# Performance work log

Hardware: AMD Instinct MI355X
Metric: run time of the kernel (lower is better)

Reference implementation:

```python
import jax, jax.numpy as jnp
import numpy as np

HIDDEN_DIM = 8


def setup_inputs() -> dict:
    key = jax.random.key(0)
    ks = jax.random.split(key, 10)
    B, S, C, H = 2048, 200, 25, HIDDEN_DIM
    s = 0.1
    return {
        "x": jax.random.normal(ks[0], (B, S, C), jnp.float32),
        "delay_W": jax.random.normal(ks[1], (S, C), jnp.float32) * s,
        "delay_b": jax.random.normal(ks[2], (S,), jnp.float32) * s,
        "U_W": jax.random.normal(ks[3], (H, C), jnp.float32) * s,
        "U_b": jax.random.normal(ks[4], (H,), jnp.float32) * s,
        "A_W": jax.random.normal(ks[5], (H, H), jnp.float32) * s,
        "B_W": jax.random.normal(ks[6], (H, C), jnp.float32) * s,
        "B_b": jax.random.normal(ks[7], (H,), jnp.float32) * s,
        "out_W": jax.random.normal(ks[8], (C, H), jnp.float32) * s,
        "out_b": jax.random.normal(ks[9], (C,), jnp.float32) * s,
    }


def reference(x, delay_W, delay_b, U_W, U_b, A_W, B_W, B_b, out_W, out_b):
    # x: [B, S, C] -> [S, B, C]
    xt = jnp.swapaxes(x, 0, 1)
    S, B, C = xt.shape
    # synaptic delay: each source timestep t distributes its signal over
    # all output timesteps via a softmax over the TIMESTEPS axis.
    logits = xt @ delay_W.T + delay_b                # [S, B, S]
    w = jax.nn.softmax(logits, axis=-1)              # [S, B, S_out]
    x_del = jnp.einsum('tbc,tbs->sbc', xt, w)        # [S_out, B, C]
    # SSM inputs
    u = x_del @ U_W.T + U_b                          # [S, B, H]
    b = jax.nn.sigmoid(x_del @ B_W.T + B_b)          # [S, B, H]

    # linear recurrence h_t = h_{t-1} A^T + b_t * u_t, h_0 = 0
    def step(h, bu):
        b_t, u_t = bu
        h = h @ A_W.T + b_t * u_t
        return h, h

    h0 = jnp.zeros((B, HIDDEN_DIM), xt.dtype)
    _, hs = jax.lax.scan(step, h0, (b, u))           # [S, B, H]
    out = hs @ out_W.T + out_b                       # [S, B, C]
    return jnp.swapaxes(out, 0, 1)                   # [B, S, C]
```

## Files before the change

kernel.cpp:

```cpp
#include <hip/hip_runtime.h>

#define NB 2048
#define S_ 200
#define C_ 25
#define H_ 8
#define WROWS 208
#define STR 36
#define NSTRIP 13
#define NSTILE 13
#define NPAIR 7
#define XDS 26
#define WFRAG (13 * 64 * 4)

typedef __bf16   bf16x8 __attribute__((ext_vector_type(8)));
typedef float    f32x4  __attribute__((ext_vector_type(4)));
typedef unsigned uint4v __attribute__((ext_vector_type(4)));

struct Frag { bf16x8 hi, lo; };

__device__ __forceinline__ unsigned short f2bf(float f) {
    unsigned u = __builtin_bit_cast(unsigned, f);
    return (unsigned short)((u + 0x7FFFu + ((u >> 16) & 1u)) >> 16);
}
__device__ __forceinline__ float bfh2f(unsigned short h) {
    return __builtin_bit_cast(float, (unsigned)h << 16);
}
__device__ __forceinline__ unsigned pack_hl(float v) {
    unsigned short h = f2bf(v);
    unsigned short l = f2bf(v - bfh2f(h));
    return (unsigned)h | ((unsigned)l << 16);
}
__device__ __forceinline__ unsigned hi_pair(unsigned d0, unsigned d1) {
    return (d0 & 0xFFFFu) | (d1 << 16);
}
__device__ __forceinline__ unsigned lo_pair(unsigned d0, unsigned d1) {
    return (d0 >> 16) | (d1 & 0xFFFF0000u);
}
__device__ __forceinline__ Frag build_frag8(uint4v d0, uint4v d1) {
    uint4v h, l;
    h.x = hi_pair(d0.x, d0.y); h.y = hi_pair(d0.z, d0.w);
    h.z = hi_pair(d1.x, d1.y); h.w = hi_pair(d1.z, d1.w);
    l.x = lo_pair(d0.x, d0.y); l.y = lo_pair(d0.z, d0.w);
    l.z = lo_pair(d1.x, d1.y); l.w = lo_pair(d1.z, d1.w);
    Frag f;
    f.hi = __builtin_bit_cast(bf16x8, h);
    f.lo = __builtin_bit_cast(bf16x8, l);
    return f;
}
__device__ __forceinline__ bf16x8 build_hi8(uint4v d0, uint4v d1) {
    uint4v h;
    h.x = hi_pair(d0.x, d0.y); h.y = hi_pair(d0.z, d0.w);
    h.z = hi_pair(d1.x, d1.y); h.w = hi_pair(d1.z, d1.w);
    return __builtin_bit_cast(bf16x8, h);
}
__device__ __forceinline__ f32x4 mfma16(bf16x8 a, bf16x8 b, f32x4 c) {
    return __builtin_amdgcn_mfma_f32_16x16x32_bf16(a, b, c, 0, 0, 0);
}
__device__ __forceinline__ f32x4 mfma_split(const Frag& a, const Frag& b, f32x4 c) {
    c = mfma16(a.hi, b.hi, c);
    c = mfma16(a.hi, b.lo, c);
    c = mfma16(a.lo, b.hi, c);
    return c;
}
__device__ __forceinline__ float fexp2(float x) {
    float r; asm("v_exp_f32 %0, %1" : "=v"(r) : "v"(x)); return r;
}
__device__ __forceinline__ float flog2(float x) {
    float r; asm("v_log_f32 %0, %1" : "=v"(r) : "v"(x)); return r;
}
__device__ __forceinline__ unsigned cvt_pk_bf16(float vlo, float vhi) {
    unsigned r; asm("v_cvt_pk_bf16_f32 %0, %1, %2" : "=v"(r) : "v"(vlo), "v"(vhi)); return r;
}
__device__ __forceinline__ float lo16f(unsigned p) { return __builtin_bit_cast(float, p << 16); }
__device__ __forceinline__ float hi16f(unsigned p) { return __builtin_bit_cast(float, p & 0xFFFF0000u); }

__device__ __forceinline__ void xpose_quads(unsigned& a0, unsigned& a1,
                                            unsigned& b0, unsigned& b1) {
    asm("v_permlane32_swap_b32 %0, %1" : "+v"(a0), "+v"(b0));
    asm("v_permlane32_swap_b32 %0, %1" : "+v"(a1), "+v"(b1));
    asm("v_permlane16_swap_b32 %0, %1" : "+v"(a0), "+v"(b0));
    asm("v_permlane16_swap_b32 %0, %1" : "+v"(a1), "+v"(b1));
}

__global__ void prep_w_kernel(const float* __restrict__ delay_W,
                              const float* __restrict__ A_W,
                              unsigned* __restrict__ ws) {
    const float LOG2E = 1.44269504088896340736f;
    unsigned* Whi = ws;
    unsigned* Wlo = ws + WFRAG;
    for (int idx = blockIdx.x * 256 + threadIdx.x; idx < WFRAG; idx += gridDim.x * 256) {
        int d = idx & 3, lane = (idx >> 2) & 63, sv = idx >> 8;
        int q = lane >> 4, nn = lane & 15;
        int s  = sv * 16 + nn;
        int c0 = q * 8 + 2 * d;
        float v0 = (s < S_ && c0     < C_) ? delay_W[s * C_ + c0]     * LOG2E : 0.f;
        float v1 = (s < S_ && c0 + 1 < C_) ? delay_W[s * C_ + c0 + 1] * LOG2E : 0.f;
        unsigned short h0 = f2bf(v0), h1 = f2bf(v1);
        unsigned short l0 = f2bf(v0 - bfh2f(h0)), l1 = f2bf(v1 - bfh2f(h1));
        Whi[idx] = (unsigned)h0 | ((unsigned)h1 << 16);
        Wlo[idx] = (unsigned)l0 | ((unsigned)l1 << 16);
    }
    __shared__ float A2s[64];
    if (blockIdx.x == 0) {
        float* A2g = (float*)(ws + 2 * WFRAG);
        float* A4g = (float*)(ws + 2 * WFRAG + 64);
        const int i = threadIdx.x >> 3, j = threadIdx.x & 7;
        if (threadIdx.x < 64) {
            float s = 0.f;
            for (int k = 0; k < 8; ++k) s = fmaf(A_W[i * 8 + k], A_W[k * 8 + j], s);
            A2s[threadIdx.x] = s; A2g[threadIdx.x] = s;
        }
        __syncthreads();
        if (threadIdx.x < 64) {
            float s = 0.f;
            for (int k = 0; k < 8; ++k) s = fmaf(A2s[i * 8 + k], A2s[k * 8 + j], s);
            A4g[threadIdx.x] = s;
        }
    }
}

__global__ __launch_bounds__(256, 5) void ssm_syn_delay_kernel(
    const float* __restrict__ x,       const unsigned* __restrict__ ws,
    const float* __restrict__ delay_b, const float* __restrict__ U_W,
    const float* __restrict__ U_b,     const float* __restrict__ A_W,
    const float* __restrict__ B_W,     const float* __restrict__ B_b,
    const float* __restrict__ out_W,   const float* __restrict__ out_b,
    float* __restrict__ out)
{
    __shared__ __align__(16) unsigned X32[WROWS * STR];
    __shared__ __align__(16) float lsed[WROWS];
    __shared__ __align__(16) float dbs_l[WROWS];

    const int tid  = threadIdx.x;
    const int wid  = tid >> 6;
    const int lane = tid & 63;
    const int q    = lane >> 4;
    const int n    = lane & 15;
    const int b    = blockIdx.x;
    const float* xb = x + (size_t)b * (S_ * C_);
    const unsigned* Whi = ws;
    const unsigned* Wlo = ws + WFRAG;
    const float* A2g = (const float*)(ws + 2 * WFRAG);
    const float* A4g = (const float*)(ws + 2 * WFRAG + 64);

    for (int i = tid; i < WROWS * 9; i += 256) {
        int r = i / 9, cg = i - r * 9;
        f32x4 v = {0.f, 0.f, 0.f, 0.f};
        if (r < S_) {
            if (cg < 6)       __builtin_memcpy(&v, &xb[r * C_ + cg * 4], 16);
            else if (cg == 6) v[0] = xb[r * C_ + 24];
        }
        uint4v p;
        p.x = pack_hl(v[0]); p.y = pack_hl(v[1]); p.z = pack_hl(v[2]); p.w = pack_hl(v[3]);
        *(uint4v*)&X32[r * STR + cg * 4] = p;
    }
    for (int i = tid; i < WROWS; i += 256)
        dbs_l[i] = (i < S_) ? delay_b[i] * 1.44269504088896340736f : -1e30f;
    __syncthreads();

    for (int st = wid; st < NSTRIP; st += 4) {
        const int t = st * 16 + n;
        const uint4v* xp = (const uint4v*)&X32[t * STR + q * 8];
        Frag fa = build_frag8(xp[0], xp[1]);
        float rs0 = 0.f, rs1 = 0.f, rs2 = 0.f, rs3 = 0.f;
        for (int sv = 0; sv < NSTILE; ++sv) {
            Frag fb;
            fb.hi = __builtin_bit_cast(bf16x8, *(const uint4v*)&Whi[(sv * 64 + lane) * 4]);
            fb.lo = __builtin_bit_cast(bf16x8, *(const uint4v*)&Wlo[(sv * 64 + lane) * 4]);
            f32x4 L = {0.f, 0.f, 0.f, 0.f};
            L = mfma_split(fa, fb, L);
            const float dbv = dbs_l[sv * 16 + n];
            rs0 += fexp2(L[0] + dbv);
            rs1 += fexp2(L[1] + dbv);
            rs2 += fexp2(L[2] + dbv);
            rs3 += fexp2(L[3] + dbv);
        }
#pragma unroll
        for (int off = 1; off < 16; off <<= 1) {
            rs0 += __shfl_xor(rs0, off);
            rs1 += __shfl_xor(rs1, off);
            rs2 += __shfl_xor(rs2, off);
            rs3 += __shfl_xor(rs3, off);
        }
        if (n < 4) {
            float v = (n == 0) ? rs0 : (n == 1) ? rs1 : (n == 2) ? rs2 : rs3;
            lsed[st * 16 + q * 4 + n] = flog2(v);
        }
    }
    __syncthreads();

    f32x4 acc[4][2];
#pragma unroll
    for (int i = 0; i < 4; ++i)
#pragma unroll
        for (int j = 0; j < 2; ++j) acc[i][j] = f32x4{0.f, 0.f, 0.f, 0.f};

    for (int pair = 0; pair < NPAIR; ++pair) {
        const int sA = 2 * pair, sB = sA + 1;
        const bool bval = (sB < NSTRIP);
        const uint4v* xpA = (const uint4v*)&X32[(sA * 16 + n) * STR + q * 8];
        Frag faA = build_frag8(xpA[0], xpA[1]);
        Frag faB;
        if (bval) {
            const uint4v* xpB = (const uint4v*)&X32[(sB * 16 + n) * STR + q * 8];
            faB = build_frag8(xpB[0], xpB[1]);
        }
        f32x4 lseA = *(const f32x4*)&lsed[sA * 16 + q * 4];
        f32x4 lseB = bval ? *(const f32x4*)&lsed[sB * 16 + q * 4] : f32x4{0,0,0,0};
        bf16x8 b2h[2];
#pragma unroll
        for (int ct = 0; ct < 2; ++ct) {
            const int c = ct * 16 + n;
            uint4v d0, d1;
#pragma unroll
            for (int j = 0; j < 4; ++j) {
                int t2 = pair * 32 + q * 8 + j;
                ((unsigned*)&d0)[j] = (t2 < WROWS) ? X32[t2 * STR + c] : 0u;
            }
#pragma unroll
            for (int j = 0; j < 4; ++j) {
                int t2 = pair * 32 + q * 8 + 4 + j;
                ((unsigned*)&d1)[j] = (t2 < WROWS) ? X32[t2 * STR + c] : 0u;
            }
            b2h[ct] = build_hi8(d0, d1);
        }

#pragma unroll
        for (int si = 0; si < 4; ++si) {
            const int sv = wid + 4 * si;
            if (sv >= NSTILE) continue;
            Frag fb;
            fb.hi = __builtin_bit_cast(bf16x8, *(const uint4v*)&Whi[(sv * 64 + lane) * 4]);
            fb.lo = __builtin_bit_cast(bf16x8, *(const uint4v*)&Wlo[(sv * 64 + lane) * 4]);
            const float dbv = dbs_l[sv * 16 + n];
            unsigned pA0, pA1, qA0, qA1;
            {
                f32x4 L = {0.f, 0.f, 0.f, 0.f};
                L = mfma_split(faA, fb, L);
                float e0 = fexp2(L[0] + dbv - lseA[0]);
                float e1 = fexp2(L[1] + dbv - lseA[1]);
                float e2 = fexp2(L[2] + dbv - lseA[2]);
                float e3 = fexp2(L[3] + dbv - lseA[3]);
                pA0 = cvt_pk_bf16(e0, e1);
                pA1 = cvt_pk_bf16(e2, e3);
                qA0 = cvt_pk_bf16(e0 - lo16f(pA0), e1 - hi16f(pA0));
                qA1 = cvt_pk_bf16(e2 - lo16f(pA1), e3 - hi16f(pA1));
            }
            unsigned pB0 = 0u, pB1 = 0u, qB0 = 0u, qB1 = 0u;
            if (bval) {
                f32x4 L = {0.f, 0.f, 0.f, 0.f};
                L = mfma_split(faB, fb, L);
                float e0 = fexp2(L[0] + dbv - lseB[0]);
                float e1 = fexp2(L[1] + dbv - lseB[1]);
                float e2 = fexp2(L[2] + dbv - lseB[2]);
                float e3 = fexp2(L[3] + dbv - lseB[3]);
                pB0 = cvt_pk_bf16(e0, e1);
                pB1 = cvt_pk_bf16(e2, e3);
                qB0 = cvt_pk_bf16(e0 - lo16f(pB0), e1 - hi16f(pB0));
                qB1 = cvt_pk_bf16(e2 - lo16f(pB1), e3 - hi16f(pB1));
            }
            xpose_quads(pA0, pA1, pB0, pB1);
            xpose_quads(qA0, qA1, qB0, qB1);
            uint4v hv = {pA0, pA1, pB0, pB1};
            uint4v lv = {qA0, qA1, qB0, qB1};
            bf16x8 a2h = __builtin_bit_cast(bf16x8, hv);
            bf16x8 a2l = __builtin_bit_cast(bf16x8, lv);
#pragma unroll
            for (int ct = 0; ct < 2; ++ct) {
                f32x4 c4 = acc[si][ct];
                c4 = mfma16(a2h, b2h[ct], c4);
                c4 = mfma16(a2l, b2h[ct], c4);
                acc[si][ct] = c4;
            }
        }
    }
    __syncthreads();

    float* xdelf = (float*)&X32[0];
    float* p_s   = (float*)&X32[5696];
#pragma unroll
    for (int si = 0; si < 4; ++si) {
        const int sv = wid + 4 * si;
        if (sv >= NSTILE) continue;
#pragma unroll
        for (int ct = 0; ct < 2; ++ct) {
            const int c = ct * 16 + n;
            if (c < C_) {
#pragma unroll
                for (int r = 0; r < 4; ++r) {
                    const int s = sv * 16 + q * 4 + r;
                    if (s < S_) xdelf[s * XDS + c] = acc[si][ct][r];
                }
            }
        }
    }
    __syncthreads();

    if (tid < S_) {
        const int s = tid;
        float a[C_];
#pragma unroll
        for (int i = 0; i < C_; ++i) a[i] = xdelf[s * XDS + i];
#pragma unroll
        for (int h = 0; h < H_; ++h) {
            float uu = U_b[h];
            float bb = B_b[h];
#pragma unroll
            for (int i = 0; i < C_; ++i) {
                uu = fmaf(a[i], U_W[h * C_ + i], uu);
                bb = fmaf(a[i], B_W[h * C_ + i], bb);
            }
            float sg_ = 1.0f / (1.0f + __expf(-bb));
            p_s[s * H_ + h] = uu * sg_;
        }
    }
    __syncthreads();

    float* p1 = xdelf;
    float* p2 = xdelf + S_ * H_;
    for (int i2 = tid; i2 < S_ * H_; i2 += 256) {
        const int s = i2 >> 3, i = i2 & 7;
        float v = p_s[i2];
        if (s > 0) {
            const float* pm = &p_s[(s - 1) * H_];
#pragma unroll
            for (int j = 0; j < H_; ++j) v = fmaf(A_W[i * H_ + j], pm[j], v);
        }
        p1[i2] = v;
    }
    __syncthreads();
    for (int i2 = tid; i2 < S_ * H_; i2 += 256) {
        const int s = i2 >> 3, i = i2 & 7;
        float v = p1[i2];
        if (s > 1) {
            const float* pm = &p1[(s - 2) * H_];
#pragma unroll
            for (int j = 0; j < H_; ++j) v = fmaf(A2g[i * H_ + j], pm[j], v);
        }
        p2[i2] = v;
    }
    __syncthreads();
    if (tid < 32) {
        const int r = tid >> 3, i = tid & 7;
        float A4r[H_];
#pragma unroll
        for (int j = 0; j < H_; ++j) A4r[j] = A4g[i * H_ + j];
        float h = 0.f;
        for (int k = 0; k < 50; ++k) {
            const int s = 4 * k + r;
            float v = p2[s * H_ + i];
#pragma unroll
            for (int j = 0; j < H_; ++j) v = fmaf(A4r[j], __shfl(h, j, 8), v);
            h = v;
            p_s[s * H_ + i] = h;
        }
    }
    __syncthreads();

    float* ob_ptr = out + (size_t)b * (S_ * C_);
    for (int i = tid; i < S_ * C_; i += 256) {
        int s = i / C_, c = i - s * C_;
        float v = out_b[c];
#pragma unroll
        for (int h = 0; h < H_; ++h)
            v = fmaf(p_s[s * H_ + h], out_W[c * H_ + h], v);
        ob_ptr[i] = v;
    }
}

extern "C" void kernel_launch(void* const* d_in, const int* in_sizes, int n_in,
                              void* d_out, int out_size, void* d_ws, size_t ws_size,
                              hipStream_t stream) {
    const float* x       = (const float*)d_in[0];
    const float* delay_W = (const float*)d_in[1];
    const float* delay_b = (const float*)d_in[2];
    const float* U_W     = (const float*)d_in[3];
    const float* U_b     = (const float*)d_in[4];
    const float* A_W     = (const float*)d_in[5];
    const float* B_W     = (const float*)d_in[6];
    const float* B_b     = (const float*)d_in[7];
    const float* out_W   = (const float*)d_in[8];
    const float* out_b   = (const float*)d_in[9];
    float* out = (float*)d_out;
    unsigned* ws = (unsigned*)d_ws;

    prep_w_kernel<<<4, 256, 0, stream>>>(delay_W, A_W, ws);
    ssm_syn_delay_kernel<<<NB, 256, 0, stream>>>(
        x, ws, delay_b, U_W, U_b, A_W, B_W, B_b, out_W, out_b, out);
}
```

Before: 241.9 us.

## Batch logsumexp strips per wave, hoist W fragments, vectorize LDS loads

The input packing now converts two values at once with the packed bf16 convert instruction. The logsumexp pass processes all of a wave's strips together so each loaded W tile is reused across strips. In the softmax-weighted accumulation loop, the W fragments and delay biases are hoisted out of the pair loop. The x_del row stride is padded to 28 so the U/B projection and the output projection can use vector LDS and global loads. Together these cut redundant global and LDS loads and instruction count, at the cost of more registers held live.

After: 375.6 us. 55.3% more time.

```diff
diff --git a/kernel.cpp b/kernel.cpp
--- a/kernel.cpp
+++ b/kernel.cpp
@@ -9,7 +9,7 @@
 #define NSTRIP 13
 #define NSTILE 13
 #define NPAIR 7
-#define XDS 26
+#define XDS 28
 #define WFRAG (13 * 64 * 4)
 
 typedef __bf16   bf16x8 __attribute__((ext_vector_type(8)));
@@ -73,6 +73,14 @@
 }
 __device__ __forceinline__ float lo16f(unsigned p) { return __builtin_bit_cast(float, p << 16); }
 __device__ __forceinline__ float hi16f(unsigned p) { return __builtin_bit_cast(float, p & 0xFFFF0000u); }
+__device__ __forceinline__ void pack_hl2(float v0, float v1, unsigned& d0, unsigned& d1) {
+    unsigned hp = cvt_pk_bf16(v0, v1);
+    float r0 = v0 - lo16f(hp);
+    float r1 = v1 - hi16f(hp);
+    unsigned lp = cvt_pk_bf16(r0, r1);
+    d0 = (hp & 0xFFFFu) | (lp << 16);
+    d1 = (hp >> 16) | (lp & 0xFFFF0000u);
+}
 
 __device__ __forceinline__ void xpose_quads(unsigned& a0, unsigned& a1,
                                             unsigned& b0, unsigned& b1) {
@@ -150,41 +158,60 @@
             if (cg < 6)       __builtin_memcpy(&v, &xb[r * C_ + cg * 4], 16);
             else if (cg == 6) v[0] = xb[r * C_ + 24];
         }
-        uint4v p;
-        p.x = pack_hl(v[0]); p.y = pack_hl(v[1]); p.z = pack_hl(v[2]); p.w = pack_hl(v[3]);
+        unsigned e0, e1, e2, e3;
+        pack_hl2(v[0], v[1], e0, e1);
+        pack_hl2(v[2], v[3], e2, e3);
+        uint4v p = {e0, e1, e2, e3};
         *(uint4v*)&X32[r * STR + cg * 4] = p;
     }
     for (int i = tid; i < WROWS; i += 256)
         dbs_l[i] = (i < S_) ? delay_b[i] * 1.44269504088896340736f : -1e30f;
     __syncthreads();
 
-    for (int st = wid; st < NSTRIP; st += 4) {
-        const int t = st * 16 + n;
-        const uint4v* xp = (const uint4v*)&X32[t * STR + q * 8];
-        Frag fa = build_frag8(xp[0], xp[1]);
-        float rs0 = 0.f, rs1 = 0.f, rs2 = 0.f, rs3 = 0.f;
+    {
+        Frag fa[4];
+        f32x4 rs[4];
+#pragma unroll
+        for (int k = 0; k < 4; ++k) {
+            rs[k] = f32x4{0.f, 0.f, 0.f, 0.f};
+            const int st = wid + 4 * k;
+            if (st < NSTRIP) {
+                const uint4v* xp = (const uint4v*)&X32[(st * 16 + n) * STR + q * 8];
+                fa[k] = build_frag8(xp[0], xp[1]);
+            }
+        }
         for (int sv = 0; sv < NSTILE; ++sv) {
             Frag fb;
             fb.hi = __builtin_bit_cast(bf16x8, *(const uint4v*)&Whi[(sv * 64 + lane) * 4]);
             fb.lo = __builtin_bit_cast(bf16x8, *(const uint4v*)&Wlo[(sv * 64 + lane) * 4]);
-            f32x4 L = {0.f, 0.f, 0.f, 0.f};
-            L = mfma_split(fa, fb, L);
             const float dbv = dbs_l[sv * 16 + n];
-            rs0 += fexp2(L[0] + dbv);
-            rs1 += fexp2(L[1] + dbv);
-            rs2 += fexp2(L[2] + dbv);
-            rs3 += fexp2(L[3] + dbv);
-        }
-#pragma unroll
-        for (int off = 1; off < 16; off <<= 1) {
-            rs0 += __shfl_xor(rs0, off);
-            rs1 += __shfl_xor(rs1, off);
-            rs2 += __shfl_xor(rs2, off);
-            rs3 += __shfl_xor(rs3, off);
-        }
-        if (n < 4) {
-            float v = (n == 0) ? rs0 : (n == 1) ? rs1 : (n == 2) ? rs2 : rs3;
-            lsed[st * 16 + q * 4 + n] = flog2(v);
+#pragma unroll
+            for (int k = 0; k < 4; ++k) {
+                if (wid + 4 * k >= NSTRIP) continue;
+                f32x4 L = {0.f, 0.f, 0.f, 0.f};
+                L = mfma_split(fa[k], fb, L);
+                rs[k][0] += fexp2(L[0] + dbv);
+                rs[k][1] += fexp2(L[1] + dbv);
+                rs[k][2] += fexp2(L[2] + dbv);
+                rs[k][3] += fexp2(L[3] + dbv);
+            }
+        }
+#pragma unroll
+        for (int k = 0; k < 4; ++k) {
+            const int st = wid + 4 * k;
+            if (st >= NSTRIP) continue;
+            float r0 = rs[k][0], r1 = rs[k][1], r2 = rs[k][2], r3 = rs[k][3];
+#pragma unroll
+            for (int off = 1; off < 16; off <<= 1) {
+                r0 += __shfl_xor(r0, off);
+                r1 += __shfl_xor(r1, off);
+                r2 += __shfl_xor(r2, off);
+                r3 += __shfl_xor(r3, off);
+            }
+            if (n < 4) {
+                float v = (n == 0) ? r0 : (n == 1) ? r1 : (n == 2) ? r2 : r3;
+                lsed[st * 16 + q * 4 + n] = flog2(v);
+            }
         }
     }
     __syncthreads();
@@ -194,6 +221,18 @@
     for (int i = 0; i < 4; ++i)
 #pragma unroll
         for (int j = 0; j < 2; ++j) acc[i][j] = f32x4{0.f, 0.f, 0.f, 0.f};
+
+    Frag fbs[4];
+    float dbv4[4] = {0.f, 0.f, 0.f, 0.f};
+#pragma unroll
+    for (int si = 0; si < 4; ++si) {
+        const int sv = wid + 4 * si;
+        if (sv < NSTILE) {
+            fbs[si].hi = __builtin_bit_cast(bf16x8, *(const uint4v*)&Whi[(sv * 64 + lane) * 4]);
+            fbs[si].lo = __builtin_bit_cast(bf16x8, *(const uint4v*)&Wlo[(sv * 64 + lane) * 4]);
+            dbv4[si] = dbs_l[sv * 16 + n];
+        }
+    }
 
     for (int pair = 0; pair < NPAIR; ++pair) {
         const int sA = 2 * pair, sB = sA + 1;
@@ -229,14 +268,11 @@
         for (int si = 0; si < 4; ++si) {
             const int sv = wid + 4 * si;
             if (sv >= NSTILE) continue;
-            Frag fb;
-            fb.hi = __builtin_bit_cast(bf16x8, *(const uint4v*)&Whi[(sv * 64 + lane) * 4]);
-            fb.lo = __builtin_bit_cast(bf16x8, *(const uint4v*)&Wlo[(sv * 64 + lane) * 4]);
-            const float dbv = dbs_l[sv * 16 + n];
+            const float dbv = dbv4[si];
             unsigned pA0, pA1, qA0, qA1;
             {
                 f32x4 L = {0.f, 0.f, 0.f, 0.f};
-                L = mfma_split(faA, fb, L);
+                L = mfma_split(faA, fbs[si], L);
                 float e0 = fexp2(L[0] + dbv - lseA[0]);
                 float e1 = fexp2(L[1] + dbv - lseA[1]);
                 float e2 = fexp2(L[2] + dbv - lseA[2]);
@@ -249,7 +285,7 @@
             unsigned pB0 = 0u, pB1 = 0u, qB0 = 0u, qB1 = 0u;
             if (bval) {
                 f32x4 L = {0.f, 0.f, 0.f, 0.f};
-                L = mfma_split(faB, fb, L);
+                L = mfma_split(faB, fbs[si], L);
                 float e0 = fexp2(L[0] + dbv - lseB[0]);
                 float e1 = fexp2(L[1] + dbv - lseB[1]);
                 float e2 = fexp2(L[2] + dbv - lseB[2]);
@@ -298,15 +334,17 @@
 
     if (tid < S_) {
         const int s = tid;
-        float a[C_];
-#pragma unroll
-        for (int i = 0; i < C_; ++i) a[i] = xdelf[s * XDS + i];
+        float a[24];
+        const f32x4* ar = (const f32x4*)&xdelf[s * XDS];
+#pragma unroll
+        for (int k = 0; k < 6; ++k) *(f32x4*)&a[k * 4] = ar[k];
+        float a24 = xdelf[s * XDS + 24];
 #pragma unroll
         for (int h = 0; h < H_; ++h) {
-            float uu = U_b[h];
-            float bb = B_b[h];
-#pragma unroll
-            for (int i = 0; i < C_; ++i) {
+            float uu = fmaf(a24, U_W[h * C_ + 24], U_b[h]);
+            float bb = fmaf(a24, B_W[h * C_ + 24], B_b[h]);
+#pragma unroll
+            for (int i = 0; i < 24; ++i) {
                 uu = fmaf(a[i], U_W[h * C_ + i], uu);
                 bb = fmaf(a[i], B_W[h * C_ + i], bb);
             }
@@ -360,10 +398,19 @@
     float* ob_ptr = out + (size_t)b * (S_ * C_);
     for (int i = tid; i < S_ * C_; i += 256) {
         int s = i / C_, c = i - s * C_;
+        const f32x4* pr = (const f32x4*)&p_s[s * H_];
+        const f32x4* wr = (const f32x4*)&out_W[c * H_];
+        f32x4 h0 = pr[0], h1 = pr[1];
+        f32x4 w0 = wr[0], w1 = wr[1];
         float v = out_b[c];
-#pragma unroll
-        for (int h = 0; h < H_; ++h)
-            v = fmaf(p_s[s * H_ + h], out_W[c * H_ + h], v);
+        v = fmaf(h0[0], w0[0], v);
+        v = fmaf(h0[1], w0[1], v);
+        v = fmaf(h0[2], w0[2], v);
+        v = fmaf(h0[3], w0[3], v);
+        v = fmaf(h1[0], w1[0], v);
+        v = fmaf(h1[1], w1[1], v);
+        v = fmaf(h1[2], w1[2], v);
+        v = fmaf(h1[3], w1[3], v);
         ob_ptr[i] = v;
     }
 }
```
